# Performance work log

Measured on AMD Instinct MI355X. Metric: run time of the kernel, lower is better.

The kernel has to match this reference:

```python
import jax, jax.numpy as jnp
import numpy as np

EPS = 1e-6
C = 4  # actual_num_ways

def _rms(x):
    # x * rsqrt(mean(x^2, -1) + eps)
    return x * jax.lax.rsqrt(jnp.mean(x * x, axis=-1, keepdims=True) + EPS)

def setup_inputs() -> dict:
    key = jax.random.key(0)
    k1, k2, k3 = jax.random.split(key, 3)
    L, B, T, D = 12, 2, 2048, 2048
    H = C * L  # da_hidden_dim = 48
    xs = jax.random.normal(k1, (L, B, T, D), dtype=jnp.float32)
    w1 = jax.random.normal(k2, (D, H), dtype=jnp.float32) * 0.02
    w2 = jax.random.normal(k3, (H, C * L), dtype=jnp.float32) * 0.02
    static_weight = jnp.zeros((C, L), dtype=jnp.float32)
    pre_scales = jnp.ones((L, D), dtype=jnp.float32)
    post_scales = jnp.ones((C, D), dtype=jnp.float32)
    return {"xs": xs, "w1": w1, "w2": w2, "static_weight": static_weight,
            "pre_scales": pre_scales, "post_scales": post_scales}

def reference(xs, w1, w2, static_weight, pre_scales, post_scales):
    # xs: [L, B, T, D]; returns stacked ways [C, B, T, D]
    L, B, T, D = xs.shape
    x_current = xs[-1]                                   # [B,T,D]
    dw = jax.nn.gelu(_rms(x_current) @ w1, approximate=False)  # [B,T,H]
    dw = dw @ w2                                         # [B,T,C*L]
    dw = dw.reshape(B, T, C, L).transpose(2, 0, 1, 3)    # [C,B,T,L]
    dw = dw + static_weight[:, None, None, :]
    # pre-DA RMSNorm with learned scale per layer
    xs_normed = _rms(xs) * pre_scales[:, None, None, :]  # [L,B,T,D]
    agg = jnp.einsum('cbtl,lbtd->cbtd', dw, xs_normed)   # [C,B,T,D]
    # post-DA RMSNorm with learned scale per way, plus residual
    out = _rms(agg) * post_scales[:, None, None, :] + x_current[None]
    return out
```

## Files before the change

### kernel.cpp

```cpp
#include <hip/hip_runtime.h>
#include <math.h>

#define NL 12
#define NB 2
#define NT 2048
#define ND 2048
#define NC 4
#define NH 48
#define NBT (NB*NT)
#define BTD ((long)NBT*(long)ND)
#define TOK 8
#define ATOK 8
#define AGRID (NBT/ATOK)

typedef float fx4 __attribute__((ext_vector_type(4)));

__device__ __forceinline__ float gelu_exact(float x) {
    return 0.5f * x * (1.0f + erff(x * 0.70710678118654752f));
}

__global__ __launch_bounds__(256, 2)
void dw_kernel(const float* __restrict__ xs,
               const float* __restrict__ w1,
               const float* __restrict__ w2,
               const float* __restrict__ sw,
               float* __restrict__ dw_out) {
    __shared__ float xls[TOK][ND];
    __shared__ float rinv_s[TOK];
    __shared__ float y_s[TOK][NH];
    const int tid  = threadIdx.x;
    const int wave = tid >> 6;
    const int lane = tid & 63;

    const float* xcur = xs + (long)(NL - 1) * BTD + (long)blockIdx.x * TOK * ND;
    const float4* src = (const float4*)xcur;
    float4* dst = (float4*)&xls[0][0];
    #pragma unroll
    for (int i = 0; i < (TOK * ND / 4) / 256; ++i)
        dst[tid + i * 256] = src[tid + i * 256];
    __syncthreads();

    #pragma unroll
    for (int tt = 0; tt < 2; ++tt) {
        const int tok = wave * 2 + tt;
        float ss = 0.f;
        for (int d = lane; d < ND; d += 64) { float v = xls[tok][d]; ss += v * v; }
        #pragma unroll
        for (int off = 32; off; off >>= 1) ss += __shfl_xor(ss, off);
        if (lane == 0) rinv_s[tok] = rsqrtf(ss * (1.0f / ND) + 1e-6f);
    }
    __syncthreads();

    float rv[TOK];
    #pragma unroll
    for (int t = 0; t < TOK; ++t) rv[t] = rinv_s[t];

    float acc[TOK][12];
    #pragma unroll
    for (int t = 0; t < TOK; ++t)
        #pragma unroll
        for (int j = 0; j < 12; ++j) acc[t][j] = 0.f;

    const int h0 = wave * 12;
    for (int d = lane; d < ND; d += 64) {
        const float* wrow = w1 + (long)d * NH + h0;
        const float4 wA = *(const float4*)(wrow);
        const float4 wB = *(const float4*)(wrow + 4);
        const float4 wC = *(const float4*)(wrow + 8);
        #pragma unroll
        for (int t = 0; t < TOK; ++t) {
            const float xv = xls[t][d] * rv[t];
            acc[t][0]  += xv * wA.x; acc[t][1]  += xv * wA.y;
            acc[t][2]  += xv * wA.z; acc[t][3]  += xv * wA.w;
            acc[t][4]  += xv * wB.x; acc[t][5]  += xv * wB.y;
            acc[t][6]  += xv * wB.z; acc[t][7]  += xv * wB.w;
            acc[t][8]  += xv * wC.x; acc[t][9]  += xv * wC.y;
            acc[t][10] += xv * wC.z; acc[t][11] += xv * wC.w;
        }
    }
    #pragma unroll
    for (int t = 0; t < TOK; ++t)
        #pragma unroll
        for (int j = 0; j < 12; ++j) {
            float v = acc[t][j];
            #pragma unroll
            for (int off = 32; off; off >>= 1) v += __shfl_xor(v, off);
            acc[t][j] = v;
        }
    if (lane == 0) {
        #pragma unroll
        for (int t = 0; t < TOK; ++t)
            #pragma unroll
            for (int j = 0; j < 12; ++j)
                y_s[t][h0 + j] = acc[t][j];
    }
    __syncthreads();

    for (int i = tid; i < TOK * NH; i += 256) {
        float* p = &y_s[0][0];
        p[i] = gelu_exact(p[i]);
    }
    __syncthreads();

    for (int i = tid; i < TOK * NH; i += 256) {
        const int tok = i / NH;
        const int j   = i - tok * NH;
        float z = sw[j];
        #pragma unroll
        for (int h = 0; h < NH; ++h) z += y_s[tok][h] * w2[h * NH + j];
        dw_out[((long)blockIdx.x * TOK + tok) * NH + j] = z;
    }
}

__global__ __launch_bounds__(512, 4)
void agg_kernel(const float* __restrict__ xs,
                const float* __restrict__ dw,
                const float* __restrict__ pre_scales,
                const float* __restrict__ post_scales,
                float* __restrict__ out) {
    const int tid  = threadIdx.x;
    const int wave = tid >> 6;
    const int lane = tid & 63;
    const int coff = tid * 4;

    __shared__ float red[8][NL];
    __shared__ float red2[8][NC];
    __shared__ float dws[NC * NL];

    const long tok0 = (long)blockIdx.x * ATOK;

    #pragma unroll 1
    for (int t = 0; t < ATOK; ++t) {
        const long tok = tok0 + t;

        if (tid < NC * NL) {
            const int c = tid / NL, l = tid - c * NL;
            dws[l * NC + c] = dw[tok * (NC * NL) + tid];
        }

        fx4 x[NL];
        #pragma unroll
        for (int l = 0; l < NL; ++l)
            x[l] = *(const fx4*)(xs + (long)l * BTD + tok * ND + coff);

        #pragma unroll
        for (int l = 0; l < NL; ++l) {
            float v = x[l].x*x[l].x + x[l].y*x[l].y
                    + x[l].z*x[l].z + x[l].w*x[l].w;
            #pragma unroll
            for (int off = 32; off; off >>= 1) v += __shfl_xor(v, off);
            if (lane == 0) red[wave][l] = v;
        }
        __syncthreads();

        float rvv[NL];
        {
            float s[NL];
            #pragma unroll
            for (int l = 0; l < NL; ++l) s[l] = 0.f;
            #pragma unroll
            for (int w = 0; w < 8; ++w) {
                const fx4 r0 = *(const fx4*)&red[w][0];
                const fx4 r1 = *(const fx4*)&red[w][4];
                const fx4 r2 = *(const fx4*)&red[w][8];
                s[0] += r0.x; s[1]  += r0.y; s[2]  += r0.z; s[3]  += r0.w;
                s[4] += r1.x; s[5]  += r1.y; s[6]  += r1.z; s[7]  += r1.w;
                s[8] += r2.x; s[9]  += r2.y; s[10] += r2.z; s[11] += r2.w;
            }
            #pragma unroll
            for (int l = 0; l < NL; ++l) rvv[l] = rsqrtf(s[l] * (1.0f / ND) + 1e-6f);
        }

        fx4 acc0 = (fx4)(0.f), acc1 = (fx4)(0.f), acc2 = (fx4)(0.f), acc3 = (fx4)(0.f);
        #pragma unroll
        for (int l = 0; l < NL; ++l) {
            const fx4 p = *(const fx4*)(pre_scales + (long)l * ND + coff);
            const fx4 w4 = *(const fx4*)&dws[l * NC];
            const fx4 xn = x[l] * rvv[l] * p;
            acc0 += w4.x * xn;
            acc1 += w4.y * xn;
            acc2 += w4.z * xn;
            acc3 += w4.w * xn;
        }

        {
            float q0 = acc0.x*acc0.x + acc0.y*acc0.y + acc0.z*acc0.z + acc0.w*acc0.w;
            float q1 = acc1.x*acc1.x + acc1.y*acc1.y + acc1.z*acc1.z + acc1.w*acc1.w;
            float q2 = acc2.x*acc2.x + acc2.y*acc2.y + acc2.z*acc2.z + acc2.w*acc2.w;
            float q3 = acc3.x*acc3.x + acc3.y*acc3.y + acc3.z*acc3.z + acc3.w*acc3.w;
            #pragma unroll
            for (int off = 32; off; off >>= 1) {
                q0 += __shfl_xor(q0, off);
                q1 += __shfl_xor(q1, off);
                q2 += __shfl_xor(q2, off);
                q3 += __shfl_xor(q3, off);
            }
            if (lane == 0) {
                red2[wave][0] = q0; red2[wave][1] = q1;
                red2[wave][2] = q2; red2[wave][3] = q3;
            }
        }
        __syncthreads();

        float r2[NC];
        {
            float s2[NC];
            #pragma unroll
            for (int c = 0; c < NC; ++c) s2[c] = 0.f;
            #pragma unroll
            for (int w = 0; w < 8; ++w) {
                const fx4 r = *(const fx4*)&red2[w][0];
                s2[0] += r.x; s2[1] += r.y; s2[2] += r.z; s2[3] += r.w;
            }
            #pragma unroll
            for (int c = 0; c < NC; ++c) r2[c] = rsqrtf(s2[c] * (1.0f / ND) + 1e-6f);
        }

        const fx4 xcur = x[NL - 1];
        {
            const fx4 q0 = *(const fx4*)(post_scales + 0L * ND + coff);
            const fx4 q1 = *(const fx4*)(post_scales + 1L * ND + coff);
            const fx4 q2 = *(const fx4*)(post_scales + 2L * ND + coff);
            const fx4 q3 = *(const fx4*)(post_scales + 3L * ND + coff);
            const fx4 o0 = acc0 * r2[0] * q0 + xcur;
            const fx4 o1 = acc1 * r2[1] * q1 + xcur;
            const fx4 o2 = acc2 * r2[2] * q2 + xcur;
            const fx4 o3 = acc3 * r2[3] * q3 + xcur;
            __builtin_nontemporal_store(o0, (fx4*)(out + 0L * BTD + tok * ND + coff));
            __builtin_nontemporal_store(o1, (fx4*)(out + 1L * BTD + tok * ND + coff));
            __builtin_nontemporal_store(o2, (fx4*)(out + 2L * BTD + tok * ND + coff));
            __builtin_nontemporal_store(o3, (fx4*)(out + 3L * BTD + tok * ND + coff));
        }
    }
}

extern "C" void kernel_launch(void* const* d_in, const int* in_sizes, int n_in,
                              void* d_out, int out_size, void* d_ws, size_t ws_size,
                              hipStream_t stream) {
    const float* xs   = (const float*)d_in[0];
    const float* w1   = (const float*)d_in[1];
    const float* w2   = (const float*)d_in[2];
    const float* sw   = (const float*)d_in[3];
    const float* pre  = (const float*)d_in[4];
    const float* post = (const float*)d_in[5];
    float* out   = (float*)d_out;
    float* dw_ws = (float*)d_ws;

    dw_kernel<<<NBT / TOK, 256, 0, stream>>>(xs, w1, w2, sw, dw_ws);
    agg_kernel<<<AGRID, 512, 0, stream>>>(xs, dw_ws, pre, post, out);
}
```

Measured before the change: 185.1 us.

## Use one token per agg block and reload xs instead of holding in registers

The aggregation kernel now launches one block per token instead of looping over eight tokens per block. It no longer keeps all twelve layer vectors in registers between the sum-of-squares pass and the weighted-sum pass; it reads xs from global memory a second time and relies on the cache for those reloads. The aim is to cut register pressure and raise occupancy and parallelism, at the cost of roughly twice the xs load traffic through the cache hierarchy and more blocks to launch.

```diff
diff --git a/kernel.cpp b/kernel.cpp
--- a/kernel.cpp
+++ b/kernel.cpp
@@ -10,8 +10,6 @@
 #define NBT (NB*NT)
 #define BTD ((long)NBT*(long)ND)
 #define TOK 8
-#define ATOK 8
-#define AGRID (NBT/ATOK)
 
 typedef float fx4 __attribute__((ext_vector_type(4)));
 
@@ -122,115 +120,111 @@
     const int wave = tid >> 6;
     const int lane = tid & 63;
     const int coff = tid * 4;
+    const long token = blockIdx.x;
 
     __shared__ float red[8][NL];
     __shared__ float red2[8][NC];
     __shared__ float dws[NC * NL];
 
-    const long tok0 = (long)blockIdx.x * ATOK;
-
-    #pragma unroll 1
-    for (int t = 0; t < ATOK; ++t) {
-        const long tok = tok0 + t;
-
-        if (tid < NC * NL) {
-            const int c = tid / NL, l = tid - c * NL;
-            dws[l * NC + c] = dw[tok * (NC * NL) + tid];
-        }
-
-        fx4 x[NL];
-        #pragma unroll
-        for (int l = 0; l < NL; ++l)
-            x[l] = *(const fx4*)(xs + (long)l * BTD + tok * ND + coff);
-
-        #pragma unroll
-        for (int l = 0; l < NL; ++l) {
-            float v = x[l].x*x[l].x + x[l].y*x[l].y
-                    + x[l].z*x[l].z + x[l].w*x[l].w;
-            #pragma unroll
-            for (int off = 32; off; off >>= 1) v += __shfl_xor(v, off);
-            if (lane == 0) red[wave][l] = v;
-        }
-        __syncthreads();
-
-        float rvv[NL];
-        {
-            float s[NL];
-            #pragma unroll
-            for (int l = 0; l < NL; ++l) s[l] = 0.f;
-            #pragma unroll
-            for (int w = 0; w < 8; ++w) {
-                const fx4 r0 = *(const fx4*)&red[w][0];
-                const fx4 r1 = *(const fx4*)&red[w][4];
-                const fx4 r2 = *(const fx4*)&red[w][8];
-                s[0] += r0.x; s[1]  += r0.y; s[2]  += r0.z; s[3]  += r0.w;
-                s[4] += r1.x; s[5]  += r1.y; s[6]  += r1.z; s[7]  += r1.w;
-                s[8] += r2.x; s[9]  += r2.y; s[10] += r2.z; s[11] += r2.w;
-            }
-            #pragma unroll
-            for (int l = 0; l < NL; ++l) rvv[l] = rsqrtf(s[l] * (1.0f / ND) + 1e-6f);
-        }
-
-        fx4 acc0 = (fx4)(0.f), acc1 = (fx4)(0.f), acc2 = (fx4)(0.f), acc3 = (fx4)(0.f);
-        #pragma unroll
-        for (int l = 0; l < NL; ++l) {
-            const fx4 p = *(const fx4*)(pre_scales + (long)l * ND + coff);
-            const fx4 w4 = *(const fx4*)&dws[l * NC];
-            const fx4 xn = x[l] * rvv[l] * p;
-            acc0 += w4.x * xn;
-            acc1 += w4.y * xn;
-            acc2 += w4.z * xn;
-            acc3 += w4.w * xn;
-        }
-
-        {
-            float q0 = acc0.x*acc0.x + acc0.y*acc0.y + acc0.z*acc0.z + acc0.w*acc0.w;
-            float q1 = acc1.x*acc1.x + acc1.y*acc1.y + acc1.z*acc1.z + acc1.w*acc1.w;
-            float q2 = acc2.x*acc2.x + acc2.y*acc2.y + acc2.z*acc2.z + acc2.w*acc2.w;
-            float q3 = acc3.x*acc3.x + acc3.y*acc3.y + acc3.z*acc3.z + acc3.w*acc3.w;
-            #pragma unroll
-            for (int off = 32; off; off >>= 1) {
-                q0 += __shfl_xor(q0, off);
-                q1 += __shfl_xor(q1, off);
-                q2 += __shfl_xor(q2, off);
-                q3 += __shfl_xor(q3, off);
-            }
-            if (lane == 0) {
-                red2[wave][0] = q0; red2[wave][1] = q1;
-                red2[wave][2] = q2; red2[wave][3] = q3;
-            }
-        }
-        __syncthreads();
-
-        float r2[NC];
-        {
-            float s2[NC];
-            #pragma unroll
-            for (int c = 0; c < NC; ++c) s2[c] = 0.f;
-            #pragma unroll
-            for (int w = 0; w < 8; ++w) {
-                const fx4 r = *(const fx4*)&red2[w][0];
-                s2[0] += r.x; s2[1] += r.y; s2[2] += r.z; s2[3] += r.w;
-            }
-            #pragma unroll
-            for (int c = 0; c < NC; ++c) r2[c] = rsqrtf(s2[c] * (1.0f / ND) + 1e-6f);
-        }
-
-        const fx4 xcur = x[NL - 1];
-        {
-            const fx4 q0 = *(const fx4*)(post_scales + 0L * ND + coff);
-            const fx4 q1 = *(const fx4*)(post_scales + 1L * ND + coff);
-            const fx4 q2 = *(const fx4*)(post_scales + 2L * ND + coff);
-            const fx4 q3 = *(const fx4*)(post_scales + 3L * ND + coff);
-            const fx4 o0 = acc0 * r2[0] * q0 + xcur;
-            const fx4 o1 = acc1 * r2[1] * q1 + xcur;
-            const fx4 o2 = acc2 * r2[2] * q2 + xcur;
-            const fx4 o3 = acc3 * r2[3] * q3 + xcur;
-            __builtin_nontemporal_store(o0, (fx4*)(out + 0L * BTD + tok * ND + coff));
-            __builtin_nontemporal_store(o1, (fx4*)(out + 1L * BTD + tok * ND + coff));
-            __builtin_nontemporal_store(o2, (fx4*)(out + 2L * BTD + tok * ND + coff));
-            __builtin_nontemporal_store(o3, (fx4*)(out + 3L * BTD + tok * ND + coff));
-        }
+    if (tid < NC * NL) {
+        const int c = tid / NL, l = tid - c * NL;
+        dws[l * NC + c] = dw[token * (NC * NL) + tid];
+    }
+
+    float ss[NL];
+    fx4 xcur;
+    #pragma unroll
+    for (int l = 0; l < NL; ++l) {
+        const fx4 v = *(const fx4*)(xs + (long)l * BTD + token * ND + coff);
+        ss[l] = v.x*v.x + v.y*v.y + v.z*v.z + v.w*v.w;
+        if (l == NL - 1) xcur = v;
+    }
+    #pragma unroll
+    for (int l = 0; l < NL; ++l) {
+        float v = ss[l];
+        #pragma unroll
+        for (int off = 32; off; off >>= 1) v += __shfl_xor(v, off);
+        if (lane == 0) red[wave][l] = v;
+    }
+    __syncthreads();
+
+    float rvv[NL];
+    {
+        float s[NL];
+        #pragma unroll
+        for (int l = 0; l < NL; ++l) s[l] = 0.f;
+        #pragma unroll
+        for (int w = 0; w < 8; ++w) {
+            const fx4 r0 = *(const fx4*)&red[w][0];
+            const fx4 r1 = *(const fx4*)&red[w][4];
+            const fx4 r2 = *(const fx4*)&red[w][8];
+            s[0] += r0.x; s[1]  += r0.y; s[2]  += r0.z; s[3]  += r0.w;
+            s[4] += r1.x; s[5]  += r1.y; s[6]  += r1.z; s[7]  += r1.w;
+            s[8] += r2.x; s[9]  += r2.y; s[10] += r2.z; s[11] += r2.w;
+        }
+        #pragma unroll
+        for (int l = 0; l < NL; ++l) rvv[l] = rsqrtf(s[l] * (1.0f / ND) + 1e-6f);
+    }
+
+    fx4 acc0 = (fx4)(0.f), acc1 = (fx4)(0.f), acc2 = (fx4)(0.f), acc3 = (fx4)(0.f);
+    #pragma unroll
+    for (int l = 0; l < NL; ++l) {
+        const fx4 v = *(const fx4*)(xs + (long)l * BTD + token * ND + coff);
+        const fx4 p = *(const fx4*)(pre_scales + (long)l * ND + coff);
+        const fx4 w4 = *(const fx4*)&dws[l * NC];
+        const fx4 xn = v * rvv[l] * p;
+        acc0 += w4.x * xn;
+        acc1 += w4.y * xn;
+        acc2 += w4.z * xn;
+        acc3 += w4.w * xn;
+    }
+
+    {
+        float q0 = acc0.x*acc0.x + acc0.y*acc0.y + acc0.z*acc0.z + acc0.w*acc0.w;
+        float q1 = acc1.x*acc1.x + acc1.y*acc1.y + acc1.z*acc1.z + acc1.w*acc1.w;
+        float q2 = acc2.x*acc2.x + acc2.y*acc2.y + acc2.z*acc2.z + acc2.w*acc2.w;
+        float q3 = acc3.x*acc3.x + acc3.y*acc3.y + acc3.z*acc3.z + acc3.w*acc3.w;
+        #pragma unroll
+        for (int off = 32; off; off >>= 1) {
+            q0 += __shfl_xor(q0, off);
+            q1 += __shfl_xor(q1, off);
+            q2 += __shfl_xor(q2, off);
+            q3 += __shfl_xor(q3, off);
+        }
+        if (lane == 0) {
+            red2[wave][0] = q0; red2[wave][1] = q1;
+            red2[wave][2] = q2; red2[wave][3] = q3;
+        }
+    }
+    __syncthreads();
+
+    float r2[NC];
+    {
+        float s2[NC];
+        #pragma unroll
+        for (int c = 0; c < NC; ++c) s2[c] = 0.f;
+        #pragma unroll
+        for (int w = 0; w < 8; ++w) {
+            const fx4 r = *(const fx4*)&red2[w][0];
+            s2[0] += r.x; s2[1] += r.y; s2[2] += r.z; s2[3] += r.w;
+        }
+        #pragma unroll
+        for (int c = 0; c < NC; ++c) r2[c] = rsqrtf(s2[c] * (1.0f / ND) + 1e-6f);
+    }
+
+    {
+        const fx4 q0 = *(const fx4*)(post_scales + 0L * ND + coff);
+        const fx4 q1 = *(const fx4*)(post_scales + 1L * ND + coff);
+        const fx4 q2 = *(const fx4*)(post_scales + 2L * ND + coff);
+        const fx4 q3 = *(const fx4*)(post_scales + 3L * ND + coff);
+        const fx4 o0 = acc0 * r2[0] * q0 + xcur;
+        const fx4 o1 = acc1 * r2[1] * q1 + xcur;
+        const fx4 o2 = acc2 * r2[2] * q2 + xcur;
+        const fx4 o3 = acc3 * r2[3] * q3 + xcur;
+        __builtin_nontemporal_store(o0, (fx4*)(out + 0L * BTD + token * ND + coff));
+        __builtin_nontemporal_store(o1, (fx4*)(out + 1L * BTD + token * ND + coff));
+        __builtin_nontemporal_store(o2, (fx4*)(out + 2L * BTD + token * ND + coff));
+        __builtin_nontemporal_store(o3, (fx4*)(out + 3L * BTD + token * ND + coff));
     }
 }
 
@@ -247,5 +241,5 @@
     float* dw_ws = (float*)d_ws;
 
     dw_kernel<<<NBT / TOK, 256, 0, stream>>>(xs, w1, w2, sw, dw_ws);
-    agg_kernel<<<AGRID, 512, 0, stream>>>(xs, dw_ws, pre, post, out);
-}
+    agg_kernel<<<NBT, 512, 0, stream>>>(xs, dw_ws, pre, post, out);
+}
```

New measurement: 185.6 us. No clear change (+0.3%).
